# Optimization experiments

Measured on AMD Instinct MI355X. Metric: run time of the kernel, lower is better.

## Reference

```python
import jax, jax.numpy as jnp
import numpy as np

D_MODEL = 1024
N_HEAD = 16
HEAD_DIM = D_MODEL // N_HEAD


def setup_inputs() -> dict:
    key = jax.random.key(0)
    ks = jax.random.split(key, 11)
    B, L = 1, 2048
    s = 1.0 / np.sqrt(D_MODEL)
    return {
        "q": jax.random.normal(ks[0], (B, L, D_MODEL), jnp.float32),
        "k": jax.random.normal(ks[1], (B, L, D_MODEL), jnp.float32),
        "v": jax.random.normal(ks[2], (B, L, D_MODEL), jnp.float32),
        "w_q": jax.random.normal(ks[3], (D_MODEL, D_MODEL), jnp.float32) * s,
        "b_q": jax.random.normal(ks[4], (D_MODEL,), jnp.float32) * s,
        "w_k": jax.random.normal(ks[5], (D_MODEL, D_MODEL), jnp.float32) * s,
        "b_k": jax.random.normal(ks[6], (D_MODEL,), jnp.float32) * s,
        "w_v": jax.random.normal(ks[7], (D_MODEL, D_MODEL), jnp.float32) * s,
        "b_v": jax.random.normal(ks[8], (D_MODEL,), jnp.float32) * s,
        "w_o": jax.random.normal(ks[9], (D_MODEL, D_MODEL), jnp.float32) * s,
        "b_o": jax.random.normal(ks[10], (D_MODEL,), jnp.float32) * s,
    }


def _split_heads(x):
    # [B, L, D] -> [B, H, L, Dh]
    B, L, D = x.shape
    return x.reshape(B, L, N_HEAD, HEAD_DIM).transpose(0, 2, 1, 3)


def reference(q, k, v, w_q, b_q, w_k, b_k, w_v, b_v, w_o, b_o):
    # Linear projections (torch Linear: x @ W.T + b; here weights stored as [D_in, D_out])
    qh = _split_heads(q @ w_q + b_q)
    kh = _split_heads(k @ w_k + b_k)
    vh = _split_heads(v @ w_v + b_v)
    scale = 1.0 / jnp.sqrt(jnp.asarray(HEAD_DIM, qh.dtype))
    # [B, H, Lq, Lk] full score matrix (faithful to naive implementation)
    score = jnp.einsum("bhqd,bhkd->bhqk", qh, kh) * scale
    attn = jax.nn.softmax(score, axis=-1)
    out = jnp.einsum("bhqk,bhkd->bhqd", attn, vh)
    # concat heads: [B, H, L, Dh] -> [B, L, D]
    B, H, L, Dh = out.shape
    out = out.transpose(0, 2, 1, 3).reshape(B, L, H * Dh)
    return out @ w_o + b_o  # dropout p=0.0 -> identity
```

## Files before the change

### kernel.cpp

```cpp
#include <hip/hip_runtime.h>
#include <hip/hip_bf16.h>
#include <stdint.h>
#include <stddef.h>

typedef __bf16 bf16_t;
typedef __bf16 v8bf __attribute__((ext_vector_type(8)));
typedef __bf16 v4bf __attribute__((ext_vector_type(4)));
typedef float  v4f  __attribute__((ext_vector_type(4)));

#define L_SEQ 2048
#define DM    1024
#define NH    16
#define LOG2E 1.44269504088896340736f
#define SCL   (0.125f * LOG2E)

__device__ __forceinline__ void async_cp16(const void* g, void* l) {
  __builtin_amdgcn_global_load_lds(
      (__attribute__((address_space(1))) void*)(g),
      (__attribute__((address_space(3))) void*)(l),
      16, 0, 0);
}

__device__ __forceinline__ v4f mfma16(v8bf a, v8bf b, v4f c) {
  return __builtin_amdgcn_mfma_f32_16x16x32_bf16(a, b, c, 0, 0, 0);
}

#if __has_builtin(__builtin_amdgcn_exp2f)
__device__ __forceinline__ float fast_exp2(float x) { return __builtin_amdgcn_exp2f(x); }
#else
__device__ __forceinline__ float fast_exp2(float x) { return exp2f(x); }
#endif

__global__ void k_prep(
    const float* __restrict__ q, const float* __restrict__ k,
    const float* __restrict__ v,
    const float* __restrict__ w0, const float* __restrict__ w1,
    const float* __restrict__ w2, const float* __restrict__ w3,
    bf16_t* __restrict__ Qb, bf16_t* __restrict__ Kb, bf16_t* __restrict__ Vb,
    bf16_t* __restrict__ o0, bf16_t* __restrict__ o1,
    bf16_t* __restrict__ o2, bf16_t* __restrict__ o3)
{
  const int z = blockIdx.z;
  const int tid = threadIdx.x;
  if (z < 4) {
    const float* in = (z == 0) ? w0 : (z == 1) ? w1 : (z == 2) ? w2 : w3;
    bf16_t*     out = (z == 0) ? o0 : (z == 1) ? o1 : (z == 2) ? o2 : o3;
    __shared__ float t[64 * 65];
    const int r0 = blockIdx.y * 64, c0 = blockIdx.x * 64;
#pragma unroll
    for (int p = 0; p < 16; ++p) {
      const int idx = p * 256 + tid;
      const int r = idx >> 6, c = idx & 63;
      t[r * 65 + c] = in[(size_t)(r0 + r) * DM + c0 + c];
    }
    __syncthreads();
#pragma unroll
    for (int p = 0; p < 4; ++p) {
      const int idx = p * 256 + tid;
      const int c  = idx >> 4;
      const int r4 = (idx & 15) * 4;
      v4bf y;
#pragma unroll
      for (int j = 0; j < 4; ++j) y[j] = (bf16_t)t[(r4 + j) * 65 + c];
      *(v4bf*)(&out[(size_t)(c0 + c) * DM + r0 + r4]) = y;
    }
  } else {
    const float* src = (z == 4) ? q : (z == 5) ? k : v;
    bf16_t*      dst = (z == 4) ? Qb : (z == 5) ? Kb : Vb;
    const int n4 = (L_SEQ * DM) / 4;
    const int base = (blockIdx.y * 16 + blockIdx.x) * 256 + tid;
#pragma unroll
    for (int i = base; i < n4; i += 16 * 16 * 256) {
      v4f x = ((const v4f*)src)[i];
      v4bf y;
      y[0] = (bf16_t)x[0]; y[1] = (bf16_t)x[1];
      y[2] = (bf16_t)x[2]; y[3] = (bf16_t)x[3];
      ((v4bf*)dst)[i] = y;
    }
  }
}

template <int MI, typename OutT>
__device__ __forceinline__ void gemm_body(
    const bf16_t* __restrict__ A, const bf16_t* __restrict__ Bt,
    const float* __restrict__ biasN, const float* __restrict__ biasM,
    OutT* __restrict__ C, int M, int N, int K, int bx, int by)
{
  constexpr int BM = MI * 32;
  __shared__ __align__(16) bf16_t As[2][BM * 64];
  __shared__ __align__(16) bf16_t Bs[2][64 * 64];
  const int tid  = threadIdx.x;
  const int w    = tid >> 6;
  const int lane = tid & 63;
  const int l16  = lane & 15;
  const int q4   = lane >> 4;
  const int m0   = by * BM, n0 = bx * 64;
  const int wm   = (w >> 1) * (MI * 16), wn = (w & 1) * 32;
  const int lr = lane >> 3, lc = lane & 7;

  v4f acc[MI][2];
#pragma unroll
  for (int i = 0; i < MI; ++i)
#pragma unroll
    for (int j = 0; j < 2; ++j) {
      v4f z = {0.f, 0.f, 0.f, 0.f};
      acc[i][j] = z;
    }

  auto stage = [&](int k0, int buf) {
#pragma unroll
    for (int c = 0; c < MI; ++c) {
      const int row = (BM / 4) * w + 8 * c + lr;
      const int g   = lc ^ (row & 7);
      async_cp16(A + (size_t)(m0 + row) * K + k0 + g * 8,
                 &As[buf][((BM / 4) * w + 8 * c) * 64]);
    }
#pragma unroll
    for (int c = 0; c < 2; ++c) {
      const int row = 16 * w + 8 * c + lr;
      const int g   = lc ^ (row & 7);
      async_cp16(Bt + (size_t)(n0 + row) * K + k0 + g * 8,
                 &Bs[buf][(16 * w + 8 * c) * 64]);
    }
  };

  stage(0, 0);
  __syncthreads();

  const int nk = K >> 6;
  for (int kt = 0; kt < nk; ++kt) {
    if (kt + 1 < nk) stage((kt + 1) << 6, (kt + 1) & 1);
    const int buf = kt & 1;
#pragma unroll
    for (int ks = 0; ks < 2; ++ks) {
      v8bf af[MI], bf_[2];
#pragma unroll
      for (int mi = 0; mi < MI; ++mi) {
        const int row = wm + mi * 16 + l16;
        const int pc  = (4 * ks + q4) ^ (row & 7);
        af[mi] = *(const v8bf*)(&As[buf][row * 64 + pc * 8]);
      }
#pragma unroll
      for (int ni = 0; ni < 2; ++ni) {
        const int row = wn + ni * 16 + l16;
        const int pc  = (4 * ks + q4) ^ (row & 7);
        bf_[ni] = *(const v8bf*)(&Bs[buf][row * 64 + pc * 8]);
      }
#pragma unroll
      for (int mi = 0; mi < MI; ++mi)
#pragma unroll
        for (int ni = 0; ni < 2; ++ni)
          acc[mi][ni] = mfma16(af[mi], bf_[ni], acc[mi][ni]);
    }
    __syncthreads();
  }

  float bvn[2] = {0.f, 0.f};
  if (biasN) {
#pragma unroll
    for (int ni = 0; ni < 2; ++ni) bvn[ni] = biasN[n0 + wn + ni * 16 + l16];
  }
#pragma unroll
  for (int mi = 0; mi < MI; ++mi) {
#pragma unroll
    for (int r = 0; r < 4; ++r) {
      const int row = m0 + wm + mi * 16 + q4 * 4 + r;
      const float bm = biasM ? biasM[row] : 0.f;
#pragma unroll
      for (int ni = 0; ni < 2; ++ni) {
        const int col = n0 + wn + ni * 16 + l16;
        C[(size_t)row * N + col] = (OutT)(acc[mi][ni][r] + bvn[ni] + bm);
      }
    }
  }
}

__global__ __launch_bounds__(256, 3) void k_gemm_fused(
    const bf16_t* __restrict__ Qb, const bf16_t* __restrict__ Kb,
    const bf16_t* __restrict__ Vb,
    const bf16_t* __restrict__ Wqkt,
    const bf16_t* __restrict__ Wvt,
    const float* __restrict__ bq, const float* __restrict__ bk,
    const float* __restrict__ bv,
    bf16_t* __restrict__ QKo, bf16_t* __restrict__ Vtr)
{
  const int idx = blockIdx.x;
  const bf16_t *A, *Bt;
  const float *bN = nullptr, *bM = nullptr;
  bf16_t* C;
  int M, N, bx, by;
  if (idx < 512) {
    by = idx & 15; bx = idx >> 4;
    A  = (bx < 16) ? Qb : Kb;
    Bt = Wqkt;
    bN = (bx < 16) ? bq : (bk - DM);
    C  = QKo; M = L_SEQ; N = 2 * DM;
  } else {
    const int i2 = idx - 512;
    by = i2 & 7; bx = i2 >> 3;
    A  = Wvt; Bt = Vb; bM = bv;
    C  = Vtr; M = DM; N = L_SEQ;
  }
  gemm_body<4, bf16_t>(A, Bt, bN, bM, C, M, N, DM, bx, by);
}

__global__ __launch_bounds__(256, 2) void k_gemm_oproj(
    const bf16_t* __restrict__ A, const bf16_t* __restrict__ Bt,
    const float* __restrict__ bias, float* __restrict__ C)
{
  gemm_body<2, float>(A, Bt, bias, nullptr, C, L_SEQ, DM, DM,
                      blockIdx.x, blockIdx.y);
}

__global__ __launch_bounds__(256, 4) void k_attn(
    const bf16_t* __restrict__ QKp,
    const bf16_t* __restrict__ Vt,
    bf16_t* __restrict__ AO)
{
  constexpr int LD = 2 * DM;
  const int lid = blockIdx.x;
  const int hd  = (lid & 7) + 8 * ((lid >> 3) & 1);
  const int q0  = (lid >> 4) * 32;
  const int tid = threadIdx.x, w = tid >> 6, lane = tid & 63;
  const int l16 = lane & 15, q4 = lane >> 4;
  const int lr8 = lane >> 3, lc8 = lane & 7;

  __shared__ __align__(16) char smem_raw[40960];
  bf16_t* Ks = (bf16_t*)smem_raw;
  bf16_t* QP = (bf16_t*)(smem_raw + 32768);
  float* Ored = (float*)smem_raw;
  float* Lred = (float*)(smem_raw + 34816);

  const bf16_t* Qp = QKp;
  const bf16_t* Kp = QKp + DM;

  const bf16_t* pK[4];
#pragma unroll
  for (int c = 0; c < 4; ++c) {
    const int row = 32 * w + 8 * c + lr8;
    const int g   = lc8 ^ (row & 7);
    pK[c] = Kp + (size_t)row * LD + hd * 64 + g * 8;
  }
  auto stage_k = [&](int j0, int db) {
#pragma unroll
    for (int c = 0; c < 4; ++c)
      async_cp16(pK[c] + (size_t)j0 * LD,
                 Ks + db * (128 * 64) + (32 * w + 8 * c) * 64);
  };

  const bf16_t* pV[4];
#pragma unroll
  for (int dd = 0; dd < 4; ++dd)
    pV[dd] = Vt + (size_t)(hd * 64 + dd * 16 + l16) * L_SEQ + 32 * w + q4 * 8;

  {
    const int row = 8 * w + lr8;
    const int g   = lc8 ^ (row & 7);
    async_cp16(Qp + (size_t)(q0 + row) * LD + hd * 64 + g * 8,
               QP + (8 * w) * 64);
  }
  stage_k(0, 0);
  __syncthreads();

  v8bf bq[2][2];
#pragma unroll
  for (int qg = 0; qg < 2; ++qg)
#pragma unroll
    for (int ks = 0; ks < 2; ++ks) {
      const int row = qg * 16 + l16;
      const int pc  = (4 * ks + q4) ^ (row & 7);
      bq[qg][ks] = *(const v8bf*)(&QP[row * 64 + pc * 8]);
    }
  __syncthreads();

  bf16_t* Pw = QP + w * (32 * 32);

  float l_acc[2] = {0.f, 0.f};
  v4f od[4][2];
#pragma unroll
  for (int i = 0; i < 4; ++i)
#pragma unroll
    for (int j = 0; j < 2; ++j) { v4f z = {0.f, 0.f, 0.f, 0.f}; od[i][j] = z; }

  for (int rt = 0; rt < L_SEQ / 128; ++rt) {
    v8bf av[4];
#pragma unroll
    for (int dd = 0; dd < 4; ++dd) av[dd] = *(const v8bf*)(pV[dd] + rt * 128);
    if (rt + 1 < L_SEQ / 128) stage_k((rt + 1) * 128, (rt + 1) & 1);
    const bf16_t* Kt = Ks + (rt & 1) * (128 * 64);

    v4f st[2][2];
    __builtin_amdgcn_s_setprio(1);
#pragma unroll
    for (int jf = 0; jf < 2; ++jf) {
#pragma unroll
      for (int qg = 0; qg < 2; ++qg) { v4f z = {0.f, 0.f, 0.f, 0.f}; st[jf][qg] = z; }
#pragma unroll
      for (int ks = 0; ks < 2; ++ks) {
        const int rowk = 32 * w + jf * 16 + l16;
        const int pc   = (4 * ks + q4) ^ (rowk & 7);
        v8bf ak = *(const v8bf*)(&Kt[rowk * 64 + pc * 8]);
#pragma unroll
        for (int qg = 0; qg < 2; ++qg)
          st[jf][qg] = mfma16(ak, bq[qg][ks], st[jf][qg]);
      }
    }
    __builtin_amdgcn_s_setprio(0);

#pragma unroll
    for (int jf = 0; jf < 2; ++jf)
#pragma unroll
      for (int qg = 0; qg < 2; ++qg) {
        v4bf pb;
#pragma unroll
        for (int r = 0; r < 4; ++r) {
          const float p = fast_exp2(st[jf][qg][r] * SCL);
          l_acc[qg] += p;
          pb[r] = (bf16_t)p;
        }
        const int q    = qg * 16 + l16;
        const int cch  = jf * 2 + (q4 >> 1);
        const int phys = cch ^ (q & 3);
        *(v4bf*)(&Pw[q * 32 + phys * 8 + (q4 & 1) * 4]) = pb;
      }

    __builtin_amdgcn_s_setprio(1);
#pragma unroll
    for (int qg = 0; qg < 2; ++qg) {
      const int q    = qg * 16 + l16;
      const int phys = q4 ^ (q & 3);
      v8bf bp = *(const v8bf*)(&Pw[q * 32 + phys * 8]);
#pragma unroll
      for (int dd = 0; dd < 4; ++dd)
        od[dd][qg] = mfma16(av[dd], bp, od[dd][qg]);
    }
    __builtin_amdgcn_s_setprio(0);
    __syncthreads();
  }

  float* Ow = Ored + w * (32 * 68);
#pragma unroll
  for (int dd = 0; dd < 4; ++dd)
#pragma unroll
    for (int qg = 0; qg < 2; ++qg) {
      const int q  = qg * 16 + l16;
      const int d0 = dd * 16 + q4 * 4;
      *(v4f*)(&Ow[q * 68 + d0]) = od[dd][qg];
    }
#pragma unroll
  for (int qg = 0; qg < 2; ++qg) {
    float t = l_acc[qg];
    t += __shfl_xor(t, 16, 64);
    t += __shfl_xor(t, 32, 64);
    if (q4 == 0) Lred[w * 32 + qg * 16 + l16] = t;
  }
  __syncthreads();

  const int qq = 8 * w + (lane >> 3);
  const int d0 = (lane & 7) * 8;
  const float linv =
      1.f / (Lred[qq] + Lred[32 + qq] + Lred[64 + qq] + Lred[96 + qq]);
  float o[8];
#pragma unroll
  for (int c = 0; c < 2; ++c) {
    v4f t = *(const v4f*)(&Ored[qq * 68 + d0 + c * 4]);
#pragma unroll
    for (int e = 0; e < 4; ++e) o[c * 4 + e] = t[e];
  }
#pragma unroll
  for (int w2 = 1; w2 < 4; ++w2)
#pragma unroll
    for (int c = 0; c < 2; ++c) {
      v4f t = *(const v4f*)(&Ored[w2 * (32 * 68) + qq * 68 + d0 + c * 4]);
#pragma unroll
      for (int e = 0; e < 4; ++e) o[c * 4 + e] += t[e];
    }
  v8bf ob;
#pragma unroll
  for (int e = 0; e < 8; ++e) ob[e] = (bf16_t)(o[e] * linv);
  *(v8bf*)(&AO[(size_t)(q0 + qq) * DM + hd * 64 + d0]) = ob;
}

extern "C" void kernel_launch(void* const* d_in, const int* in_sizes, int n_in,
                              void* d_out, int out_size, void* d_ws, size_t ws_size,
                              hipStream_t stream)
{
  const float* q  = (const float*)d_in[0];
  const float* k  = (const float*)d_in[1];
  const float* v  = (const float*)d_in[2];
  const float* wq = (const float*)d_in[3];
  const float* bq = (const float*)d_in[4];
  const float* wk = (const float*)d_in[5];
  const float* bk = (const float*)d_in[6];
  const float* wv = (const float*)d_in[7];
  const float* bv = (const float*)d_in[8];
  const float* wo = (const float*)d_in[9];
  const float* bo = (const float*)d_in[10];
  float* out = (float*)d_out;

  const size_t SZ = (size_t)L_SEQ * DM;
  bf16_t* ws   = (bf16_t*)d_ws;
  bf16_t* Qb   = ws;
  bf16_t* Kb   = Qb + SZ;
  bf16_t* Vb   = Kb + SZ;
  bf16_t* QK   = Vb + SZ;
  bf16_t* Vtr  = QK + 2 * SZ;
  bf16_t* AO   = Vtr + SZ;
  bf16_t* Wqt  = AO + SZ;
  bf16_t* Wkt  = Wqt + (size_t)DM * DM;
  bf16_t* Wvt  = Wkt + (size_t)DM * DM;
  bf16_t* Wot  = Wvt + (size_t)DM * DM;

  k_prep<<<dim3(16, 16, 7), 256, 0, stream>>>(q, k, v, wq, wk, wv, wo,
                                              Qb, Kb, Vb, Wqt, Wkt, Wvt, Wot);
  k_gemm_fused<<<dim3(768), 256, 0, stream>>>(Qb, Kb, Vb, Wqt, Wvt,
                                              bq, bk, bv, QK, Vtr);
  k_attn<<<dim3(1024), 256, 0, stream>>>(QK, Vtr, AO);
  k_gemm_oproj<<<dim3(16, 32), 256, 0, stream>>>(AO, Wot, bo, out);
}
```

Measured before the change: 179.6 us.

## Use 4-slot async ring pipeline in GEMMs and 64-query attention tiles

```diff
diff --git a/kernel.cpp b/kernel.cpp
--- a/kernel.cpp
+++ b/kernel.cpp
@@ -81,14 +81,15 @@
 }
 
 template <int MI, typename OutT>
-__device__ __forceinline__ void gemm_body(
+__device__ __forceinline__ void gemm_ring(
     const bf16_t* __restrict__ A, const bf16_t* __restrict__ Bt,
     const float* __restrict__ biasN, const float* __restrict__ biasM,
-    OutT* __restrict__ C, int M, int N, int K, int bx, int by)
-{
-  constexpr int BM = MI * 32;
-  __shared__ __align__(16) bf16_t As[2][BM * 64];
-  __shared__ __align__(16) bf16_t Bs[2][64 * 64];
+    OutT* __restrict__ C, int N, int K, int bx, int by)
+{
+  constexpr int BM  = MI * 32;
+  constexpr int AUW = BM / 64;
+  __shared__ __align__(16) bf16_t As[4][BM * 32];
+  __shared__ __align__(16) bf16_t Bs[4][64 * 32];
   const int tid  = threadIdx.x;
   const int w    = tid >> 6;
   const int lane = tid & 63;
@@ -96,63 +97,65 @@
   const int q4   = lane >> 4;
   const int m0   = by * BM, n0 = bx * 64;
   const int wm   = (w >> 1) * (MI * 16), wn = (w & 1) * 32;
-  const int lr = lane >> 3, lc = lane & 7;
+  const int sr   = lane >> 2, sc = lane & 3;
 
   v4f acc[MI][2];
 #pragma unroll
   for (int i = 0; i < MI; ++i)
 #pragma unroll
-    for (int j = 0; j < 2; ++j) {
-      v4f z = {0.f, 0.f, 0.f, 0.f};
-      acc[i][j] = z;
-    }
-
-  auto stage = [&](int k0, int buf) {
-#pragma unroll
-    for (int c = 0; c < MI; ++c) {
-      const int row = (BM / 4) * w + 8 * c + lr;
-      const int g   = lc ^ (row & 7);
-      async_cp16(A + (size_t)(m0 + row) * K + k0 + g * 8,
-                 &As[buf][((BM / 4) * w + 8 * c) * 64]);
-    }
-#pragma unroll
-    for (int c = 0; c < 2; ++c) {
-      const int row = 16 * w + 8 * c + lr;
-      const int g   = lc ^ (row & 7);
-      async_cp16(Bt + (size_t)(n0 + row) * K + k0 + g * 8,
-                 &Bs[buf][(16 * w + 8 * c) * 64]);
+    for (int j = 0; j < 2; ++j) { v4f z = {0.f, 0.f, 0.f, 0.f}; acc[i][j] = z; }
+
+  auto stage = [&](int s) {
+    const int slot = s & 3, k0 = s << 5;
+#pragma unroll
+    for (int c = 0; c < AUW; ++c) {
+      const int u   = w * AUW + c;
+      const int row = u * 16 + sr;
+      const int g   = sc ^ (row & 3);
+      async_cp16(A + (size_t)(m0 + row) * K + k0 + g * 8, &As[slot][u * 512]);
+    }
+    {
+      const int row = w * 16 + sr;
+      const int g   = sc ^ (row & 3);
+      async_cp16(Bt + (size_t)(n0 + row) * K + k0 + g * 8, &Bs[slot][w * 512]);
     }
   };
 
-  stage(0, 0);
-  __syncthreads();
-
-  const int nk = K >> 6;
-  for (int kt = 0; kt < nk; ++kt) {
-    if (kt + 1 < nk) stage((kt + 1) << 6, (kt + 1) & 1);
-    const int buf = kt & 1;
-#pragma unroll
-    for (int ks = 0; ks < 2; ++ks) {
-      v8bf af[MI], bf_[2];
-#pragma unroll
-      for (int mi = 0; mi < MI; ++mi) {
-        const int row = wm + mi * 16 + l16;
-        const int pc  = (4 * ks + q4) ^ (row & 7);
-        af[mi] = *(const v8bf*)(&As[buf][row * 64 + pc * 8]);
-      }
-#pragma unroll
-      for (int ni = 0; ni < 2; ++ni) {
-        const int row = wn + ni * 16 + l16;
-        const int pc  = (4 * ks + q4) ^ (row & 7);
-        bf_[ni] = *(const v8bf*)(&Bs[buf][row * 64 + pc * 8]);
-      }
-#pragma unroll
-      for (int mi = 0; mi < MI; ++mi)
-#pragma unroll
-        for (int ni = 0; ni < 2; ++ni)
-          acc[mi][ni] = mfma16(af[mi], bf_[ni], acc[mi][ni]);
-    }
-    __syncthreads();
+  stage(0); stage(1); stage(2);
+  const int NK = K >> 5;
+  for (int s = 0; s < NK; ++s) {
+    if (s < NK - 2) {
+      if constexpr (MI == 4) asm volatile("s_waitcnt vmcnt(6)" ::: "memory");
+      else                   asm volatile("s_waitcnt vmcnt(4)" ::: "memory");
+    } else if (s == NK - 2) {
+      if constexpr (MI == 4) asm volatile("s_waitcnt vmcnt(3)" ::: "memory");
+      else                   asm volatile("s_waitcnt vmcnt(2)" ::: "memory");
+    } else {
+      asm volatile("s_waitcnt vmcnt(0)" ::: "memory");
+    }
+    asm volatile("s_barrier" ::: "memory");
+    if (s + 3 < NK) stage(s + 3);
+
+    const int slot = s & 3;
+    v8bf af[MI], bfr[2];
+#pragma unroll
+    for (int mi = 0; mi < MI; ++mi) {
+      const int row = wm + mi * 16 + l16;
+      const int p   = q4 ^ (row & 3);
+      af[mi] = *(const v8bf*)(&As[slot][row * 32 + p * 8]);
+    }
+#pragma unroll
+    for (int ni = 0; ni < 2; ++ni) {
+      const int row = wn + ni * 16 + l16;
+      const int p   = q4 ^ (row & 3);
+      bfr[ni] = *(const v8bf*)(&Bs[slot][row * 32 + p * 8]);
+    }
+#pragma unroll
+    for (int mi = 0; mi < MI; ++mi)
+#pragma unroll
+      for (int ni = 0; ni < 2; ++ni)
+        acc[mi][ni] = mfma16(af[mi], bfr[ni], acc[mi][ni]);
+    __builtin_amdgcn_sched_barrier(0);
   }
 
   float bvn[2] = {0.f, 0.f};
@@ -185,34 +188,27 @@
     bf16_t* __restrict__ QKo, bf16_t* __restrict__ Vtr)
 {
   const int idx = blockIdx.x;
-  const bf16_t *A, *Bt;
-  const float *bN = nullptr, *bM = nullptr;
-  bf16_t* C;
-  int M, N, bx, by;
   if (idx < 512) {
-    by = idx & 15; bx = idx >> 4;
-    A  = (bx < 16) ? Qb : Kb;
-    Bt = Wqkt;
-    bN = (bx < 16) ? bq : (bk - DM);
-    C  = QKo; M = L_SEQ; N = 2 * DM;
+    const int by = idx & 15, bx = idx >> 4;
+    const bf16_t* A  = (bx < 16) ? Qb : Kb;
+    const float*  bN = (bx < 16) ? bq : (bk - DM);
+    gemm_ring<4, bf16_t>(A, Wqkt, bN, nullptr, QKo, 2 * DM, DM, bx, by);
   } else {
     const int i2 = idx - 512;
-    by = i2 & 7; bx = i2 >> 3;
-    A  = Wvt; Bt = Vb; bM = bv;
-    C  = Vtr; M = DM; N = L_SEQ;
-  }
-  gemm_body<4, bf16_t>(A, Bt, bN, bM, C, M, N, DM, bx, by);
+    const int by = i2 & 7, bx = i2 >> 3;
+    gemm_ring<4, bf16_t>(Wvt, Vb, nullptr, bv, Vtr, L_SEQ, DM, bx, by);
+  }
 }
 
 __global__ __launch_bounds__(256, 2) void k_gemm_oproj(
     const bf16_t* __restrict__ A, const bf16_t* __restrict__ Bt,
     const float* __restrict__ bias, float* __restrict__ C)
 {
-  gemm_body<2, float>(A, Bt, bias, nullptr, C, L_SEQ, DM, DM,
+  gemm_ring<2, float>(A, Bt, bias, nullptr, C, DM, DM,
                       blockIdx.x, blockIdx.y);
 }
 
-__global__ __launch_bounds__(256, 4) void k_attn(
+__global__ __launch_bounds__(256, 3) void k_attn(
     const bf16_t* __restrict__ QKp,
     const bf16_t* __restrict__ Vt,
     bf16_t* __restrict__ AO)
@@ -220,16 +216,14 @@
   constexpr int LD = 2 * DM;
   const int lid = blockIdx.x;
   const int hd  = (lid & 7) + 8 * ((lid >> 3) & 1);
-  const int q0  = (lid >> 4) * 32;
+  const int q0  = (lid >> 4) * 64;
   const int tid = threadIdx.x, w = tid >> 6, lane = tid & 63;
   const int l16 = lane & 15, q4 = lane >> 4;
   const int lr8 = lane >> 3, lc8 = lane & 7;
 
-  __shared__ __align__(16) char smem_raw[40960];
+  __shared__ __align__(16) char smem_raw[49152];
   bf16_t* Ks = (bf16_t*)smem_raw;
   bf16_t* QP = (bf16_t*)(smem_raw + 32768);
-  float* Ored = (float*)smem_raw;
-  float* Lred = (float*)(smem_raw + 34816);
 
   const bf16_t* Qp = QKp;
   const bf16_t* Kp = QKp + DM;
@@ -253,18 +247,19 @@
   for (int dd = 0; dd < 4; ++dd)
     pV[dd] = Vt + (size_t)(hd * 64 + dd * 16 + l16) * L_SEQ + 32 * w + q4 * 8;
 
-  {
-    const int row = 8 * w + lr8;
+#pragma unroll
+  for (int c = 0; c < 2; ++c) {
+    const int row = 16 * w + 8 * c + lr8;
     const int g   = lc8 ^ (row & 7);
     async_cp16(Qp + (size_t)(q0 + row) * LD + hd * 64 + g * 8,
-               QP + (8 * w) * 64);
+               QP + (16 * w + 8 * c) * 64);
   }
   stage_k(0, 0);
   __syncthreads();
 
-  v8bf bq[2][2];
-#pragma unroll
-  for (int qg = 0; qg < 2; ++qg)
+  v8bf bq[4][2];
+#pragma unroll
+  for (int qg = 0; qg < 4; ++qg)
 #pragma unroll
     for (int ks = 0; ks < 2; ++ks) {
       const int row = qg * 16 + l16;
@@ -273,14 +268,14 @@
     }
   __syncthreads();
 
-  bf16_t* Pw = QP + w * (32 * 32);
-
-  float l_acc[2] = {0.f, 0.f};
-  v4f od[4][2];
+  bf16_t* Pw = QP + w * (64 * 32);
+
+  float l_acc[4] = {0.f, 0.f, 0.f, 0.f};
+  v4f od[4][4];
 #pragma unroll
   for (int i = 0; i < 4; ++i)
 #pragma unroll
-    for (int j = 0; j < 2; ++j) { v4f z = {0.f, 0.f, 0.f, 0.f}; od[i][j] = z; }
+    for (int j = 0; j < 4; ++j) { v4f z = {0.f, 0.f, 0.f, 0.f}; od[i][j] = z; }
 
   for (int rt = 0; rt < L_SEQ / 128; ++rt) {
     v8bf av[4];
@@ -289,19 +284,19 @@
     if (rt + 1 < L_SEQ / 128) stage_k((rt + 1) * 128, (rt + 1) & 1);
     const bf16_t* Kt = Ks + (rt & 1) * (128 * 64);
 
-    v4f st[2][2];
+    v4f st[2][4];
     __builtin_amdgcn_s_setprio(1);
 #pragma unroll
     for (int jf = 0; jf < 2; ++jf) {
 #pragma unroll
-      for (int qg = 0; qg < 2; ++qg) { v4f z = {0.f, 0.f, 0.f, 0.f}; st[jf][qg] = z; }
+      for (int qg = 0; qg < 4; ++qg) { v4f z = {0.f, 0.f, 0.f, 0.f}; st[jf][qg] = z; }
 #pragma unroll
       for (int ks = 0; ks < 2; ++ks) {
         const int rowk = 32 * w + jf * 16 + l16;
         const int pc   = (4 * ks + q4) ^ (rowk & 7);
         v8bf ak = *(const v8bf*)(&Kt[rowk * 64 + pc * 8]);
 #pragma unroll
-        for (int qg = 0; qg < 2; ++qg)
+        for (int qg = 0; qg < 4; ++qg)
           st[jf][qg] = mfma16(ak, bq[qg][ks], st[jf][qg]);
       }
     }
@@ -310,7 +305,7 @@
 #pragma unroll
     for (int jf = 0; jf < 2; ++jf)
 #pragma unroll
-      for (int qg = 0; qg < 2; ++qg) {
+      for (int qg = 0; qg < 4; ++qg) {
         v4bf pb;
 #pragma unroll
         for (int r = 0; r < 4; ++r) {
@@ -326,7 +321,7 @@
 
     __builtin_amdgcn_s_setprio(1);
 #pragma unroll
-    for (int qg = 0; qg < 2; ++qg) {
+    for (int qg = 0; qg < 4; ++qg) {
       const int q    = qg * 16 + l16;
       const int phys = q4 ^ (q & 3);
       v8bf bp = *(const v8bf*)(&Pw[q * 32 + phys * 8]);
@@ -338,47 +333,54 @@
     __syncthreads();
   }
 
-  float* Ow = Ored + w * (32 * 68);
-#pragma unroll
-  for (int dd = 0; dd < 4; ++dd)
-#pragma unroll
-    for (int qg = 0; qg < 2; ++qg) {
-      const int q  = qg * 16 + l16;
-      const int d0 = dd * 16 + q4 * 4;
-      *(v4f*)(&Ow[q * 68 + d0]) = od[dd][qg];
-    }
-#pragma unroll
-  for (int qg = 0; qg < 2; ++qg) {
+  float* Ored = (float*)smem_raw;
+  float* Lred = (float*)(smem_raw + 34816);
+#pragma unroll
+  for (int qg = 0; qg < 4; ++qg) {
     float t = l_acc[qg];
     t += __shfl_xor(t, 16, 64);
     t += __shfl_xor(t, 32, 64);
-    if (q4 == 0) Lred[w * 32 + qg * 16 + l16] = t;
-  }
-  __syncthreads();
-
-  const int qq = 8 * w + (lane >> 3);
-  const int d0 = (lane & 7) * 8;
-  const float linv =
-      1.f / (Lred[qq] + Lred[32 + qq] + Lred[64 + qq] + Lred[96 + qq]);
-  float o[8];
-#pragma unroll
-  for (int c = 0; c < 2; ++c) {
-    v4f t = *(const v4f*)(&Ored[qq * 68 + d0 + c * 4]);
-#pragma unroll
-    for (int e = 0; e < 4; ++e) o[c * 4 + e] = t[e];
-  }
-#pragma unroll
-  for (int w2 = 1; w2 < 4; ++w2)
-#pragma unroll
-    for (int c = 0; c < 2; ++c) {
-      v4f t = *(const v4f*)(&Ored[w2 * (32 * 68) + qq * 68 + d0 + c * 4]);
-#pragma unroll
-      for (int e = 0; e < 4; ++e) o[c * 4 + e] += t[e];
-    }
+    if (q4 == 0) Lred[w * 64 + qg * 16 + l16] = t;
+  }
+  const int tq = tid >> 2;
+  const int td = (tid & 3) * 8;
+  float linv = 0.f;
+  float o[2][8];
+#pragma unroll
+  for (int H = 0; H < 2; ++H) {
+    if (H) __syncthreads();
+    float* Ow = Ored + w * (64 * 34);
+#pragma unroll
+    for (int dh = 0; dh < 2; ++dh) {
+      const int dd = 2 * H + dh;
+#pragma unroll
+      for (int qg = 0; qg < 4; ++qg) {
+        const int q = qg * 16 + l16;
+        *(v4f*)(&Ow[q * 34 + dh * 16 + q4 * 4]) = od[dd][qg];
+      }
+    }
+    __syncthreads();
+    if (H == 0)
+      linv = 1.f / (Lred[tq] + Lred[64 + tq] + Lred[128 + tq] + Lred[192 + tq]);
+#pragma unroll
+    for (int e = 0; e < 8; ++e) o[H][e] = 0.f;
+#pragma unroll
+    for (int w2 = 0; w2 < 4; ++w2)
+#pragma unroll
+      for (int c = 0; c < 2; ++c) {
+        v4f t = *(const v4f*)(&Ored[w2 * (64 * 34) + tq * 34 + td + c * 4]);
+#pragma unroll
+        for (int e = 0; e < 4; ++e) o[H][c * 4 + e] += t[e];
+      }
+  }
+  bf16_t* dst = &AO[(size_t)(q0 + tq) * DM + hd * 64];
   v8bf ob;
 #pragma unroll
-  for (int e = 0; e < 8; ++e) ob[e] = (bf16_t)(o[e] * linv);
-  *(v8bf*)(&AO[(size_t)(q0 + qq) * DM + hd * 64 + d0]) = ob;
+  for (int e = 0; e < 8; ++e) ob[e] = (bf16_t)(o[0][e] * linv);
+  *(v8bf*)(dst + td) = ob;
+#pragma unroll
+  for (int e = 0; e < 8; ++e) ob[e] = (bf16_t)(o[1][e] * linv);
+  *(v8bf*)(dst + 32 + td) = ob;
 }
 
 extern "C" void kernel_launch(void* const* d_in, const int* in_sizes, int n_in,
@@ -415,6 +417,6 @@
                                               Qb, Kb, Vb, Wqt, Wkt, Wvt, Wot);
   k_gemm_fused<<<dim3(768), 256, 0, stream>>>(Qb, Kb, Vb, Wqt, Wvt,
                                               bq, bk, bv, QK, Vtr);
-  k_attn<<<dim3(1024), 256, 0, stream>>>(QK, Vtr, AO);
+  k_attn<<<dim3(512), 256, 0, stream>>>(QK, Vtr, AO);
   k_gemm_oproj<<<dim3(16, 32), 256, 0, stream>>>(AO, Wot, bo, out);
 }
```

After: 182.3 us. No clear change (+1.5%).
